# Performance work log

Measured on AMD Instinct MI355X. Metric: run time of the kernel, lower is better.

Reference implementation:

```python
import jax, jax.numpy as jnp
import numpy as np


def _parallel_scan_affine(log_a, b):
    """Hillis-Steele doubling scan for h_t = a_t*h_{t-1} + b_t (h_0 = 0).

    log_a, b: (B, T, d). Operator: (la2,b2) o (la1,b1) = (la1+la2, exp(la2)*b1 + b2).
    """
    T = log_a.shape[1]
    la, bv = log_a, b
    stride = 1
    while stride < T:  # static Python loop, log2(T) rounds
        la_prev = jnp.roll(la, stride, axis=1).at[:, :stride, :].set(0.0)
        bv_prev = jnp.roll(bv, stride, axis=1).at[:, :stride, :].set(0.0)
        bv = jnp.exp(la) * bv_prev + bv
        la = la + la_prev
        stride *= 2
    return bv


def setup_inputs() -> dict:
    key = jax.random.key(0)
    kx, kwz, kwh = jax.random.split(key, 3)
    B, T, D = 4, 4096, 1024
    x = jax.random.normal(kx, (B, T, D), dtype=jnp.float32)
    # nn.Linear(D, D) weights, stored as (out, in) like torch
    Wz = jax.random.normal(kwz, (D, D), dtype=jnp.float32) * 0.02
    bz = jnp.zeros((D,), dtype=jnp.float32)
    Wh = jax.random.normal(kwh, (D, D), dtype=jnp.float32) * 0.02
    bh = jnp.zeros((D,), dtype=jnp.float32)
    return {"x": x, "Wz": Wz, "bz": bz, "Wh": Wh, "bh": bh}


def reference(x, Wz, bz, Wh, bh):
    # forward_parallel: z = sigmoid(linear_z(x)); h_tilde = linear_h(x)
    z = jax.nn.sigmoid(jnp.einsum("btd,ed->bte", x, Wz) + bz)
    h_tilde = jnp.einsum("btd,ed->bte", x, Wh) + bh
    log_a = jnp.log(1.0 - z + 1e-08)
    b = z * h_tilde
    h_out = _parallel_scan_affine(log_a, b)
    return h_out  # out_proj is Identity since d_inner == d_model
```

## Files before the change

kernel.cpp:

```cpp
#include <hip/hip_runtime.h>
#include <hip/hip_bf16.h>


typedef __bf16 bf16x8 __attribute__((ext_vector_type(8)));
typedef float  f32x4  __attribute__((ext_vector_type(4)));

#define BSZ 4
#define TSZ 4096
#define DSZ 1024
#define MSZ (BSZ*TSZ)
#define CH  16
#define NC  (TSZ/CH)
#define CPB 32
#define NBLK 1024

__device__ __forceinline__ void gload_lds16(const __bf16* g, __bf16* l) {
  __builtin_amdgcn_global_load_lds(
      (const __attribute__((address_space(1))) void*)g,
      (__attribute__((address_space(3))) void*)l, 16, 0, 0);
}

__device__ __forceinline__ void  spineWr(float* p, float v) {
  (void)__hip_atomic_exchange(p, v, __ATOMIC_RELAXED, __HIP_MEMORY_SCOPE_AGENT);
}
__device__ __forceinline__ float spineRd(float* p) {
  return __hip_atomic_fetch_add(p, 0.0f, __ATOMIC_RELAXED, __HIP_MEMORY_SCOPE_AGENT);
}
__device__ __forceinline__ void  flagWr(int* p, int v) {
  (void)__hip_atomic_exchange(p, v, __ATOMIC_RELAXED, __HIP_MEMORY_SCOPE_AGENT);
}
__device__ __forceinline__ int   flagRd(int* p) {
  return __hip_atomic_fetch_add(p, 0, __ATOMIC_RELAXED, __HIP_MEMORY_SCOPE_AGENT);
}

__global__ void convert_tile_kernel(const float* __restrict__ X,
                                    const float* __restrict__ Wz,
                                    const float* __restrict__ Wh,
                                    __bf16* __restrict__ Xc,
                                    __bf16* __restrict__ Wzc,
                                    __bf16* __restrict__ Whc,
                                    int* __restrict__ ctrl)
{
  const int bx = blockIdx.x;
  if (bx == 0) {
    #pragma unroll
    for (int k = 0; k < 4; ++k) ctrl[k*256 + threadIdx.x] = 0;
    if (threadIdx.x == 0) ctrl[NBLK] = 0;
  }
  const float* src; __bf16* dst; int gid;
  if (bx < 8192)      { src = X;  dst = Xc;  gid =  bx        *256 + threadIdx.x; }
  else if (bx < 8704) { src = Wz; dst = Wzc; gid = (bx - 8192)*256 + threadIdx.x; }
  else                { src = Wh; dst = Whc; gid = (bx - 8704)*256 + threadIdx.x; }
  const int l    = gid & 63;
  const int i    = (gid >> 6) & 7;
  const int kblk = (gid >> 9) & 31;
  const int rblk = gid >> 14;
  const int row  = rblk*128 + i*16 + (l & 15);
  const int col  = kblk*32 + (l >> 4)*8;
  const float* g = src + (size_t)row*DSZ + col;
  float4 v0 = *(const float4*)g;
  float4 v1 = *(const float4*)(g + 4);
  bf16x8 p;
  p[0]=(__bf16)v0.x; p[1]=(__bf16)v0.y; p[2]=(__bf16)v0.z; p[3]=(__bf16)v0.w;
  p[4]=(__bf16)v1.x; p[5]=(__bf16)v1.y; p[6]=(__bf16)v1.z; p[7]=(__bf16)v1.w;
  *(bf16x8*)(dst + (size_t)gid*8) = p;
}

__global__ __launch_bounds__(256, 2) void gemm_scan_kernel(
    const __bf16* __restrict__ Xc,  const __bf16* __restrict__ Wzc,
    const __bf16* __restrict__ Whc,
    const float* __restrict__ bz, const float* __restrict__ bh,
    float* __restrict__ out,
    float* aggA, float* aggB, float* incA, float* incB, int* ctrl)
{
  __shared__ __align__(16) __bf16 As [8192];
  __shared__ __align__(16) __bf16 Bzs[8192];
  __shared__ __align__(16) __bf16 Bhs[8192];
  __shared__ int vbid_s;

  const int tid  = threadIdx.x;
  if (tid == 0)
    vbid_s = __hip_atomic_fetch_add(&ctrl[NBLK], 1, __ATOMIC_RELAXED,
                                    __HIP_MEMORY_SCOPE_AGENT) & (NBLK - 1);
  __syncthreads();
  const int vbid = vbid_s;
  const int bx = vbid >> 3;
  const int by = vbid & 7;

  const int lane = tid & 63;
  const int wv   = tid >> 6;
  const int wM   = (wv >> 1) * 64;
  const int wN   = (wv & 1) * 64;
  const int wMg  = wM >> 4;
  const int wNg  = wN >> 4;
  const int lr   = lane & 15;
  const int q    = lane >> 4;
  const int wr   = wv >> 1;
  const int wbase = wv * 64;

  const __bf16* Xb = Xc  + (size_t)bx * 32 * 4096;
  const __bf16* Zb = Wzc + (size_t)by * 32 * 4096;
  const __bf16* Hb = Whc + (size_t)by * 32 * 4096;

  f32x4 accz[4][4] = {};
  f32x4 acch[4][4] = {};

  for (int kblk = 0; kblk < 16; ++kblk) {
    __syncthreads();
    const size_t tb = (size_t)kblk * 8192;
    #pragma unroll
    for (int c = 0; c < 4; ++c) {
      const int eo = (c*256 + wbase + lane) * 8;
      const int lo = (c*256 + wbase) * 8;
      gload_lds16(Xb + tb + eo, As  + lo);
      gload_lds16(Zb + tb + eo, Bzs + lo);
      gload_lds16(Hb + tb + eo, Bhs + lo);
    }
    __syncthreads();

    #pragma unroll
    for (int h = 0; h < 2; ++h) {
      const int ho = h * 4096;
      bf16x8 af[4];
      #pragma unroll
      for (int i = 0; i < 4; ++i)
        af[i] = *(const bf16x8*)(As + ho + (wMg + i)*512 + lane*8);
      #pragma unroll
      for (int j = 0; j < 4; ++j) {
        bf16x8 bz8 = *(const bf16x8*)(Bzs + ho + (wNg + j)*512 + lane*8);
        bf16x8 bh8 = *(const bf16x8*)(Bhs + ho + (wNg + j)*512 + lane*8);
        #pragma unroll
        for (int i = 0; i < 4; ++i) {
          accz[j][i] = __builtin_amdgcn_mfma_f32_16x16x32_bf16(af[i], bz8, accz[j][i], 0, 0, 0);
          acch[j][i] = __builtin_amdgcn_mfma_f32_16x16x32_bf16(af[i], bh8, acch[j][i], 0, 0, 0);
        }
      }
    }
  }

  const int M0 = bx * 128, N0 = by * 128;
  const int cb = bx & ~(CPB-1);
  const int fidx = vbid;

  __syncthreads();
  float* ldsA = (float*)As;
  float* ldsB = ldsA + 1024;
  float* hsL  = ldsB + 1024;

  float EA[4][4], EB[4][4];
  #pragma unroll
  for (int j = 0; j < 4; ++j) {
    const int e = N0 + wN + j*16 + lr;
    const float bzv = bz[e];
    const float bhv = bh[e];
    #pragma unroll
    for (int i = 0; i < 4; ++i) {
      float A = 1.0f, Bv = 0.0f;
      #pragma unroll
      for (int r = 0; r < 4; ++r) {
        const float pz = accz[j][i][r] + bzv;
        const float ph = acch[j][i][r] + bhv;
        const float ex = __expf(-pz);
        const float z  = 1.0f / (1.0f + ex);
        const float af = fmaf(ex, z, 1e-8f);
        const float bf = z * ph;
        Bv = fmaf(af, Bv, bf);
        A *= af;
      }
      float sA = A, sB = Bv;
      #pragma unroll
      for (int s = 16; s < 64; s <<= 1) {
        const float Ap = __shfl_up(sA, s, 64);
        const float Bp = __shfl_up(sB, s, 64);
        if (lane >= s) { sB = fmaf(sA, Bp, sB); sA *= Ap; }
      }
      float eA = __shfl_up(sA, 16, 64);
      float eB = __shfl_up(sB, 16, 64);
      if (q == 0) { eA = 1.0f; eB = 0.0f; }
      EA[j][i] = eA; EB[j][i] = eB;
      const float cA = __shfl(sA, 48 + lr, 64);
      const float cB = __shfl(sB, 48 + lr, 64);
      if (q == 0) {
        ldsA[(wr*4 + i)*128 + (e - N0)] = cA;
        ldsB[(wr*4 + i)*128 + (e - N0)] = cB;
      }
    }
  }
  __syncthreads();

  float bA[4], bB[4];
  if (wr == 1 && q == 0) {
    #pragma unroll
    for (int j = 0; j < 4; ++j) {
      const int dl = wN + j*16 + lr;
      float A = 1.0f, Bv = 0.0f;
      #pragma unroll
      for (int c = 0; c < 8; ++c) {
        const float cA = ldsA[c*128 + dl];
        const float cB = ldsB[c*128 + dl];
        Bv = fmaf(cA, Bv, cB);
        A *= cA;
      }
      bA[j] = A; bB[j] = Bv;
      const size_t sidx = (size_t)fidx*128 + dl;
      spineWr(&aggA[sidx], A);
      spineWr(&aggB[sidx], Bv);
    }
  }
  __syncthreads();
  if (tid == 0) flagWr(&ctrl[fidx], 1);

  if (wr == 1 && q == 0) {
    float Aex[4] = {1.f,1.f,1.f,1.f}, Bex[4] = {0.f,0.f,0.f,0.f};
    for (int kx = bx - 1; kx >= cb; --kx) {
      const int k = kx*8 + by;
      int f;
      do {
        f = flagRd(&ctrl[k]);
        f = __builtin_amdgcn_readfirstlane(f);
        if (f == 0) __builtin_amdgcn_s_sleep(16);
      } while (f == 0);
      float* pA = (f == 2) ? incA : aggA;
      float* pB = (f == 2) ? incB : aggB;
      #pragma unroll
      for (int j = 0; j < 4; ++j) {
        const int dl = wN + j*16 + lr;
        const size_t sidx = (size_t)k*128 + dl;
        const float kA = spineRd(&pA[sidx]);
        const float kB = spineRd(&pB[sidx]);
        Bex[j] = fmaf(Aex[j], kB, Bex[j]);
        Aex[j] *= kA;
      }
      if (f == 2) break;
    }
    #pragma unroll
    for (int j = 0; j < 4; ++j) {
      const int dl = wN + j*16 + lr;
      const size_t sidx = (size_t)fidx*128 + dl;
      spineWr(&incA[sidx], Aex[j]*bA[j]);
      spineWr(&incB[sidx], fmaf(bA[j], Bex[j], bB[j]));
      float h = Bex[j];
      #pragma unroll
      for (int c = 0; c < 8; ++c) {
        hsL[c*128 + dl] = h;
        h = fmaf(ldsA[c*128 + dl], h, ldsB[c*128 + dl]);
      }
    }
  }
  __syncthreads();
  if (tid == 0) flagWr(&ctrl[fidx], 2);

  #pragma unroll
  for (int j = 0; j < 4; ++j) {
    const int e = N0 + wN + j*16 + lr;
    const float bzv = bz[e];
    const float bhv = bh[e];
    #pragma unroll
    for (int i = 0; i < 4; ++i) {
      const int mbase = M0 + wM + i*16 + q*4;
      const float hs = hsL[(wr*4 + i)*128 + (e - N0)];
      float A = 1.0f, Bv = 0.0f;
      #pragma unroll
      for (int r = 0; r < 4; ++r) {
        const float pz = accz[j][i][r] + bzv;
        const float ph = acch[j][i][r] + bhv;
        const float ex = __expf(-pz);
        const float z  = 1.0f / (1.0f + ex);
        const float af = fmaf(ex, z, 1e-8f);
        const float bf = z * ph;
        Bv = fmaf(af, Bv, bf);
        A *= af;
        const float Apre = A * EA[j][i];
        const float Bpre = fmaf(A, EB[j][i], Bv);
        out[(size_t)(mbase + r)*DSZ + e] = fmaf(Apre, hs, Bpre);
      }
    }
  }
}

extern "C" void kernel_launch(void* const* d_in, const int* in_sizes, int n_in,
                              void* d_out, int out_size, void* d_ws, size_t ws_size,
                              hipStream_t stream)
{
  const float* x  = (const float*)d_in[0];
  const float* Wz = (const float*)d_in[1];
  const float* bz = (const float*)d_in[2];
  const float* Wh = (const float*)d_in[3];
  const float* bh = (const float*)d_in[4];
  float* out = (float*)d_out;

  __bf16* Xc   = (__bf16*)d_ws;
  __bf16* Wzc  = Xc  + (size_t)MSZ * DSZ;
  __bf16* Whc  = Wzc + (size_t)DSZ * DSZ;
  float*  aggA = (float*)(Whc + (size_t)DSZ * DSZ);
  float*  aggB = aggA + (size_t)NBLK*128;
  float*  incA = aggB + (size_t)NBLK*128;
  float*  incB = incA + (size_t)NBLK*128;
  int*    ctrl = (int*)(incB + (size_t)NBLK*128);

  convert_tile_kernel<<<9216, 256, 0, stream>>>(x, Wz, Wh, Xc, Wzc, Whc, ctrl);
  gemm_scan_kernel<<<dim3(128, 8), 256, 0, stream>>>(
      Xc, Wzc, Whc, bz, bh, out, aggA, aggB, incA, incB, ctrl);
}
```

Before: 224.8 us.

## Double-buffer LDS K-tiles and reorder block mapping to M-fastest

The GEMM main loop now splits the LDS buffers into two halves and prefetches the next K-slice while MFMAs consume the current one. This hides global-to-LDS load latency behind compute and cuts one barrier per K-step, at the cost of halving the per-step K depth. The virtual block id mapping also changes so consecutive blocks walk along M (time) for a fixed N column. The decoupled-lookback flag index is updated to match, so predecessor chunks in the scan are dispatched earlier and spin waits should shorten, while L2 reuse of the weight tiles changes.

After: 251.9 us. 12.0% more time.

```diff
diff --git a/kernel.cpp b/kernel.cpp
--- a/kernel.cpp
+++ b/kernel.cpp
@@ -84,8 +84,8 @@
                                     __HIP_MEMORY_SCOPE_AGENT) & (NBLK - 1);
   __syncthreads();
   const int vbid = vbid_s;
-  const int bx = vbid >> 3;
-  const int by = vbid & 7;
+  const int bx = vbid & 127;
+  const int by = vbid >> 7;
 
   const int lane = tid & 63;
   const int wv   = tid >> 6;
@@ -105,37 +105,45 @@
   f32x4 accz[4][4] = {};
   f32x4 acch[4][4] = {};
 
-  for (int kblk = 0; kblk < 16; ++kblk) {
+  const int eo0 = (wbase + lane) * 8;
+  const int eo1 = (256 + wbase + lane) * 8;
+  const int lo0 = wbase * 8;
+  const int lo1 = (256 + wbase) * 8;
+
+  {
+    gload_lds16(Xb + eo0, As  + lo0);  gload_lds16(Xb + eo1, As  + lo1);
+    gload_lds16(Zb + eo0, Bzs + lo0);  gload_lds16(Zb + eo1, Bzs + lo1);
+    gload_lds16(Hb + eo0, Bhs + lo0);  gload_lds16(Hb + eo1, Bhs + lo1);
+  }
+  __syncthreads();
+
+  for (int kb = 0; kb < 32; ++kb) {
+    const int cur = (kb & 1) * 4096;
+    const int nxt = cur ^ 4096;
+    if (kb < 31) {
+      const size_t g = (size_t)(kb + 1) * 4096;
+      gload_lds16(Xb + g + eo0, As  + nxt + lo0);
+      gload_lds16(Xb + g + eo1, As  + nxt + lo1);
+      gload_lds16(Zb + g + eo0, Bzs + nxt + lo0);
+      gload_lds16(Zb + g + eo1, Bzs + nxt + lo1);
+      gload_lds16(Hb + g + eo0, Bhs + nxt + lo0);
+      gload_lds16(Hb + g + eo1, Bhs + nxt + lo1);
+    }
+    bf16x8 af[4];
+    #pragma unroll
+    for (int i = 0; i < 4; ++i)
+      af[i] = *(const bf16x8*)(As + cur + (wMg + i)*512 + lane*8);
+    #pragma unroll
+    for (int j = 0; j < 4; ++j) {
+      bf16x8 bz8 = *(const bf16x8*)(Bzs + cur + (wNg + j)*512 + lane*8);
+      bf16x8 bh8 = *(const bf16x8*)(Bhs + cur + (wNg + j)*512 + lane*8);
+      #pragma unroll
+      for (int i = 0; i < 4; ++i) {
+        accz[j][i] = __builtin_amdgcn_mfma_f32_16x16x32_bf16(af[i], bz8, accz[j][i], 0, 0, 0);
+        acch[j][i] = __builtin_amdgcn_mfma_f32_16x16x32_bf16(af[i], bh8, acch[j][i], 0, 0, 0);
+      }
+    }
     __syncthreads();
-    const size_t tb = (size_t)kblk * 8192;
-    #pragma unroll
-    for (int c = 0; c < 4; ++c) {
-      const int eo = (c*256 + wbase + lane) * 8;
-      const int lo = (c*256 + wbase) * 8;
-      gload_lds16(Xb + tb + eo, As  + lo);
-      gload_lds16(Zb + tb + eo, Bzs + lo);
-      gload_lds16(Hb + tb + eo, Bhs + lo);
-    }
-    __syncthreads();
-
-    #pragma unroll
-    for (int h = 0; h < 2; ++h) {
-      const int ho = h * 4096;
-      bf16x8 af[4];
-      #pragma unroll
-      for (int i = 0; i < 4; ++i)
-        af[i] = *(const bf16x8*)(As + ho + (wMg + i)*512 + lane*8);
-      #pragma unroll
-      for (int j = 0; j < 4; ++j) {
-        bf16x8 bz8 = *(const bf16x8*)(Bzs + ho + (wNg + j)*512 + lane*8);
-        bf16x8 bh8 = *(const bf16x8*)(Bhs + ho + (wNg + j)*512 + lane*8);
-        #pragma unroll
-        for (int i = 0; i < 4; ++i) {
-          accz[j][i] = __builtin_amdgcn_mfma_f32_16x16x32_bf16(af[i], bz8, accz[j][i], 0, 0, 0);
-          acch[j][i] = __builtin_amdgcn_mfma_f32_16x16x32_bf16(af[i], bh8, acch[j][i], 0, 0, 0);
-        }
-      }
-    }
   }
 
   const int M0 = bx * 128, N0 = by * 128;
@@ -213,7 +221,7 @@
   if (wr == 1 && q == 0) {
     float Aex[4] = {1.f,1.f,1.f,1.f}, Bex[4] = {0.f,0.f,0.f,0.f};
     for (int kx = bx - 1; kx >= cb; --kx) {
-      const int k = kx*8 + by;
+      const int k = by*128 + kx;
       int f;
       do {
         f = flagRd(&ctrl[k]);
```
